# Kernel tuning notes

Hardware: AMD Instinct MI355X
Metric: run time of the kernel (lower is better)

The kernel has to match this reference:

```python
import jax, jax.numpy as jnp
import numpy as np

ALPHA = 0.5
EPS = 1e-6


def setup_inputs() -> dict:
    key = jax.random.key(0)
    k1, k2, k3 = jax.random.split(key, 3)
    B, N = 8192, 4096
    y_pred = jax.random.uniform(k1, (B, N), dtype=jnp.float32)
    y_true = jax.random.randint(k2, (B, N), 0, 2).astype(jnp.float32)
    depth_weights = jax.random.uniform(k3, (B, N), dtype=jnp.float32)
    return {"y_pred": y_pred, "y_true": y_true, "depth_weights": depth_weights}


def reference(y_pred, y_true, depth_weights):
    B, N = y_true.shape
    # --- weighted BCE ---
    bce = -(y_true * jnp.log(y_pred + EPS) + (1.0 - y_true) * jnp.log(1.0 - y_pred + EPS))
    wbce = jnp.mean(depth_weights * bce)

    # --- continuity-weighted loss: max run of correct predictions per row ---
    y_bin = (y_pred > 0.5).astype(y_true.dtype)
    correct = (y_bin == y_true)  # bool [B, N]
    idx = jnp.arange(N, dtype=jnp.int32)
    # position (1-based) of most recent incorrect element; 0 if none yet
    reset = jnp.where(correct, 0, idx + 1)  # [B, N]
    last_reset = jax.lax.cummax(reset, axis=1)  # [B, N]
    streak = (idx + 1)[None, :] - last_reset  # current run length at each position
    max_streak = jnp.max(streak, axis=1).astype(jnp.float32)  # [B]
    cwl = jnp.mean(1.0 - max_streak / N)

    return ALPHA * wbce + (1.0 - ALPHA) * cwl
```

## Files before the change

### kernel.cpp

```cpp
#include <hip/hip_runtime.h>

#define EPS 1e-6f
#define LN2F 0.69314718055994530942f

struct RunStats { int len, pre, suf, mx; };

__device__ inline RunStats rcombine(const RunStats& a, const RunStats& b) {
    RunStats r;
    r.len = a.len + b.len;
    r.pre = (a.pre == a.len) ? (a.len + b.pre) : a.pre;
    r.suf = (b.suf == b.len) ? (b.len + a.suf) : b.suf;
    r.mx  = max(max(a.mx, b.mx), a.suf + b.pre);
    return r;
}

__global__ __launch_bounds__(256) void row_kernel(
        const float* __restrict__ yp, const float* __restrict__ yt,
        const float* __restrict__ dw,
        float* __restrict__ row_wbce, int* __restrict__ row_streak) {
    const int row  = blockIdx.x;
    const int lane = threadIdx.x & 63;
    const int wave = threadIdx.x >> 6;
    const long base = (long)row * 4096 + wave * 1024 + lane * 4;

    const float4* pp = (const float4*)(yp + base);
    const float4* tp = (const float4*)(yt + base);
    const float4* wp = (const float4*)(dw + base);

    float4 P[4], T[4], W[4];
    #pragma unroll
    for (int q = 0; q < 4; ++q) {
        P[q] = pp[q * 64];
        T[q] = tp[q * 64];
        W[q] = wp[q * 64];
    }

    float sum = 0.0f;
    unsigned nibs = 0;
    #pragma unroll
    for (int q = 0; q < 4; ++q) {
        const float pv[4] = {P[q].x, P[q].y, P[q].z, P[q].w};
        const float tv[4] = {T[q].x, T[q].y, T[q].z, T[q].w};
        const float wv[4] = {W[q].x, W[q].y, W[q].z, W[q].w};
        #pragma unroll
        for (int c = 0; c < 4; ++c) {
            const bool tb = tv[c] != 0.0f;
            const float sel = tb ? pv[c] : 1.0f - pv[c];
            sum = fmaf(wv[c], __log2f(sel + EPS), sum);
            const bool correct = (pv[c] > 0.5f) == tb;
            nibs |= (unsigned)correct << (8 * q + c);
        }
    }

    __shared__ unsigned nibbuf[256];
    nibbuf[wave * 64 + lane] = nibs;
    __syncthreads();
    const uint4 d = *(const uint4*)&nibbuf[wave * 64 + 4 * (lane & 15)];
    const int qs = (lane >> 4) * 8;
    const unsigned mask = ((d.x >> qs) & 0xFu)
                        | (((d.y >> qs) & 0xFu) << 4)
                        | (((d.z >> qs) & 0xFu) << 8)
                        | (((d.w >> qs) & 0xFu) << 12);

    const int pre = __builtin_ctz(~mask);
    const int suf = __builtin_clz(~(mask << 16));
    int mx;
    {
        const unsigned p1 = mask;
        const unsigned p2 = p1 & (p1 << 1);
        const unsigned p4 = p2 & (p2 << 2);
        const unsigned p8 = p4 & (p4 << 4);
        unsigned z; int len;
        if (p8)      { z = p8; len = 8; }
        else if (p4) { z = p4; len = 4; }
        else if (p2) { z = p2; len = 2; }
        else         { z = p1; len = 1; }
        { const unsigned t = (z << 8) & p8; if (t) { z = t; len += 8; } }
        { const unsigned t = (z << 4) & p4; if (t) { z = t; len += 4; } }
        { const unsigned t = (z << 2) & p2; if (t) { z = t; len += 2; } }
        { const unsigned t = (z << 1) & p1; if (t) { z = t; len += 1; } }
        mx = mask ? len : 0;
    }

    #pragma unroll
    for (int off = 32; off; off >>= 1) sum += __shfl_down(sum, off);

    int packed = pre | (suf << 10) | (mx << 20);
    int alen = 16;
    #pragma unroll
    for (int off = 1; off < 32; off <<= 1) {
        const int o = __shfl_down(packed, off);
        const int apre = packed & 1023, asuf = (packed >> 10) & 1023, amx = packed >> 20;
        const int bpre = o & 1023,      bsuf = (o >> 10) & 1023,      bmx = o >> 20;
        const int npre = (apre == alen) ? (alen + bpre) : apre;
        const int nsuf = (bsuf == alen) ? (alen + asuf) : bsuf;
        const int nmx  = max(max(amx, bmx), asuf + bpre);
        packed = npre | (nsuf << 10) | (nmx << 20);
        alen <<= 1;
    }
    RunStats g;
    {
        const int o = __shfl_down(packed, 32);
        const int apre = packed & 1023, asuf = (packed >> 10) & 1023, amx = packed >> 20;
        const int bpre = o & 1023,      bsuf = (o >> 10) & 1023,      bmx = o >> 20;
        g.len = 1024;
        g.pre = (apre == 512) ? (512 + bpre) : apre;
        g.suf = (bsuf == 512) ? (512 + asuf) : bsuf;
        g.mx  = max(max(amx, bmx), asuf + bpre);
    }

    __shared__ RunStats sstat[4];
    __shared__ float ssum[4];
    if (lane == 0) { sstat[wave] = g; ssum[wave] = sum; }
    __syncthreads();
    if (threadIdx.x == 0) {
        RunStats r = rcombine(rcombine(sstat[0], sstat[1]), rcombine(sstat[2], sstat[3]));
        row_wbce[row]   = -LN2F * (ssum[0] + ssum[1] + ssum[2] + ssum[3]);
        row_streak[row] = r.mx;
    }
}

__global__ __launch_bounds__(1024) void finalize_kernel(
        const float* __restrict__ row_wbce, const int* __restrict__ row_streak,
        int rows, float* __restrict__ out) {
    double s = 0.0;
    long long st = 0;
    for (int i = threadIdx.x; i < rows; i += 1024) {
        s  += (double)row_wbce[i];
        st += (long long)row_streak[i];
    }
    __shared__ double sd[1024];
    __shared__ long long sl[1024];
    sd[threadIdx.x] = s; sl[threadIdx.x] = st;
    __syncthreads();
    for (int o = 512; o; o >>= 1) {
        if (threadIdx.x < o) {
            sd[threadIdx.x] += sd[threadIdx.x + o];
            sl[threadIdx.x] += sl[threadIdx.x + o];
        }
        __syncthreads();
    }
    if (threadIdx.x == 0) {
        const double total = (double)rows * 4096.0;
        const double wbce = sd[0] / total;
        const double cwl  = 1.0 - (double)sl[0] / total;
        out[0] = (float)(0.5 * wbce + 0.5 * cwl);
    }
}

extern "C" void kernel_launch(void* const* d_in, const int* in_sizes, int n_in,
                              void* d_out, int out_size, void* d_ws, size_t ws_size,
                              hipStream_t stream) {
    const float* yp = (const float*)d_in[0];
    const float* yt = (const float*)d_in[1];
    const float* dw = (const float*)d_in[2];
    float* out = (float*)d_out;

    const int rows = in_sizes[0] / 4096;
    float* row_wbce   = (float*)d_ws;
    int*   row_streak = (int*)((char*)d_ws + (size_t)rows * sizeof(float));

    row_kernel<<<rows, 256, 0, stream>>>(yp, yt, dw, row_wbce, row_streak);
    finalize_kernel<<<1, 1024, 0, stream>>>(row_wbce, row_streak, rows, out);
}
```

Measured before the change: 348.7 us.

## Process four rows per block with register double-buffered prefetch

Each block now handles four rows and prefetches the next row's float4 loads into a second register buffer while computing the current one. This cuts block count and per-row sync/reduction overhead and aims to keep more loads in flight. The per-row __syncthreads before reading the shared nibble buffer was removed, but each wave reads only its own slice of that buffer, so this should be safe within a wave. Register pressure doubles, with launch_bounds(256,4) added, which may cause spills or lower occupancy.

```diff
diff --git a/kernel.cpp b/kernel.cpp
--- a/kernel.cpp
+++ b/kernel.cpp
@@ -2,6 +2,7 @@
 
 #define EPS 1e-6f
 #define LN2F 0.69314718055994530942f
+#define RPB 4
 
 struct RunStats { int len, pre, suf, mx; };
 
@@ -14,120 +15,141 @@
     return r;
 }
 
-__global__ __launch_bounds__(256) void row_kernel(
+__global__ __launch_bounds__(256, 4) void row_kernel(
         const float* __restrict__ yp, const float* __restrict__ yt,
         const float* __restrict__ dw,
-        float* __restrict__ row_wbce, int* __restrict__ row_streak) {
-    const int row  = blockIdx.x;
+        float* __restrict__ blk_wbce, int* __restrict__ blk_streak) {
     const int lane = threadIdx.x & 63;
     const int wave = threadIdx.x >> 6;
-    const long base = (long)row * 4096 + wave * 1024 + lane * 4;
+    const long base = (long)blockIdx.x * (RPB * 4096) + wave * 1024 + lane * 4;
 
     const float4* pp = (const float4*)(yp + base);
     const float4* tp = (const float4*)(yt + base);
     const float4* wp = (const float4*)(dw + base);
 
-    float4 P[4], T[4], W[4];
+    __shared__ unsigned nibbuf[256];
+    __shared__ RunStats sstat[RPB][4];
+    __shared__ float ssum[4];
+
+    float4 Pb[2][4], Tb[2][4], Wb[2][4];
     #pragma unroll
     for (int q = 0; q < 4; ++q) {
-        P[q] = pp[q * 64];
-        T[q] = tp[q * 64];
-        W[q] = wp[q * 64];
+        Pb[0][q] = pp[q * 64];
+        Tb[0][q] = tp[q * 64];
+        Wb[0][q] = wp[q * 64];
     }
 
     float sum = 0.0f;
-    unsigned nibs = 0;
     #pragma unroll
-    for (int q = 0; q < 4; ++q) {
-        const float pv[4] = {P[q].x, P[q].y, P[q].z, P[q].w};
-        const float tv[4] = {T[q].x, T[q].y, T[q].z, T[q].w};
-        const float wv[4] = {W[q].x, W[q].y, W[q].z, W[q].w};
+    for (int r = 0; r < RPB; ++r) {
+        const int cur = r & 1, nxt = cur ^ 1;
+        if (r + 1 < RPB) {
+            #pragma unroll
+            for (int q = 0; q < 4; ++q) {
+                Pb[nxt][q] = pp[(r + 1) * 1024 + q * 64];
+                Tb[nxt][q] = tp[(r + 1) * 1024 + q * 64];
+                Wb[nxt][q] = wp[(r + 1) * 1024 + q * 64];
+            }
+        }
+
+        unsigned nibs = 0;
         #pragma unroll
-        for (int c = 0; c < 4; ++c) {
-            const bool tb = tv[c] != 0.0f;
-            const float sel = tb ? pv[c] : 1.0f - pv[c];
-            sum = fmaf(wv[c], __log2f(sel + EPS), sum);
-            const bool correct = (pv[c] > 0.5f) == tb;
-            nibs |= (unsigned)correct << (8 * q + c);
+        for (int q = 0; q < 4; ++q) {
+            const float pv[4] = {Pb[cur][q].x, Pb[cur][q].y, Pb[cur][q].z, Pb[cur][q].w};
+            const float tv[4] = {Tb[cur][q].x, Tb[cur][q].y, Tb[cur][q].z, Tb[cur][q].w};
+            const float wv[4] = {Wb[cur][q].x, Wb[cur][q].y, Wb[cur][q].z, Wb[cur][q].w};
+            #pragma unroll
+            for (int c = 0; c < 4; ++c) {
+                const bool tb = tv[c] != 0.0f;
+                const float sel = tb ? pv[c] : 1.0f - pv[c];
+                sum = fmaf(wv[c], __log2f(sel + EPS), sum);
+                const bool correct = (pv[c] > 0.5f) == tb;
+                nibs |= (unsigned)correct << (8 * q + c);
+            }
         }
-    }
 
-    __shared__ unsigned nibbuf[256];
-    nibbuf[wave * 64 + lane] = nibs;
-    __syncthreads();
-    const uint4 d = *(const uint4*)&nibbuf[wave * 64 + 4 * (lane & 15)];
-    const int qs = (lane >> 4) * 8;
-    const unsigned mask = ((d.x >> qs) & 0xFu)
-                        | (((d.y >> qs) & 0xFu) << 4)
-                        | (((d.z >> qs) & 0xFu) << 8)
-                        | (((d.w >> qs) & 0xFu) << 12);
+        nibbuf[wave * 64 + lane] = nibs;
+        const uint4 d = *(const uint4*)&nibbuf[wave * 64 + 4 * (lane & 15)];
+        const int qs = (lane >> 4) * 8;
+        const unsigned mask = ((d.x >> qs) & 0xFu)
+                            | (((d.y >> qs) & 0xFu) << 4)
+                            | (((d.z >> qs) & 0xFu) << 8)
+                            | (((d.w >> qs) & 0xFu) << 12);
 
-    const int pre = __builtin_ctz(~mask);
-    const int suf = __builtin_clz(~(mask << 16));
-    int mx;
-    {
-        const unsigned p1 = mask;
-        const unsigned p2 = p1 & (p1 << 1);
-        const unsigned p4 = p2 & (p2 << 2);
-        const unsigned p8 = p4 & (p4 << 4);
-        unsigned z; int len;
-        if (p8)      { z = p8; len = 8; }
-        else if (p4) { z = p4; len = 4; }
-        else if (p2) { z = p2; len = 2; }
-        else         { z = p1; len = 1; }
-        { const unsigned t = (z << 8) & p8; if (t) { z = t; len += 8; } }
-        { const unsigned t = (z << 4) & p4; if (t) { z = t; len += 4; } }
-        { const unsigned t = (z << 2) & p2; if (t) { z = t; len += 2; } }
-        { const unsigned t = (z << 1) & p1; if (t) { z = t; len += 1; } }
-        mx = mask ? len : 0;
+        const int pre = __builtin_ctz(~mask);
+        const int suf = __builtin_clz(~(mask << 16));
+        int mx;
+        {
+            const unsigned p1 = mask;
+            const unsigned p2 = p1 & (p1 << 1);
+            const unsigned p4 = p2 & (p2 << 2);
+            const unsigned p8 = p4 & (p4 << 4);
+            unsigned z; int len;
+            if (p8)      { z = p8; len = 8; }
+            else if (p4) { z = p4; len = 4; }
+            else if (p2) { z = p2; len = 2; }
+            else         { z = p1; len = 1; }
+            { const unsigned t = (z << 8) & p8; if (t) { z = t; len += 8; } }
+            { const unsigned t = (z << 4) & p4; if (t) { z = t; len += 4; } }
+            { const unsigned t = (z << 2) & p2; if (t) { z = t; len += 2; } }
+            { const unsigned t = (z << 1) & p1; if (t) { z = t; len += 1; } }
+            mx = mask ? len : 0;
+        }
+
+        int packed = pre | (suf << 10) | (mx << 20);
+        int alen = 16;
+        #pragma unroll
+        for (int off = 1; off < 32; off <<= 1) {
+            const int o = __shfl_down(packed, off);
+            const int apre = packed & 1023, asuf = (packed >> 10) & 1023, amx = packed >> 20;
+            const int bpre = o & 1023,      bsuf = (o >> 10) & 1023,      bmx = o >> 20;
+            const int npre = (apre == alen) ? (alen + bpre) : apre;
+            const int nsuf = (bsuf == alen) ? (alen + asuf) : bsuf;
+            const int nmx  = max(max(amx, bmx), asuf + bpre);
+            packed = npre | (nsuf << 10) | (nmx << 20);
+            alen <<= 1;
+        }
+        {
+            const int o = __shfl_down(packed, 32);
+            const int apre = packed & 1023, asuf = (packed >> 10) & 1023, amx = packed >> 20;
+            const int bpre = o & 1023,      bsuf = (o >> 10) & 1023,      bmx = o >> 20;
+            if (lane == 0) {
+                RunStats g;
+                g.len = 1024;
+                g.pre = (apre == 512) ? (512 + bpre) : apre;
+                g.suf = (bsuf == 512) ? (512 + asuf) : bsuf;
+                g.mx  = max(max(amx, bmx), asuf + bpre);
+                sstat[r][wave] = g;
+            }
+        }
     }
 
     #pragma unroll
     for (int off = 32; off; off >>= 1) sum += __shfl_down(sum, off);
+    if (lane == 0) ssum[wave] = sum;
 
-    int packed = pre | (suf << 10) | (mx << 20);
-    int alen = 16;
-    #pragma unroll
-    for (int off = 1; off < 32; off <<= 1) {
-        const int o = __shfl_down(packed, off);
-        const int apre = packed & 1023, asuf = (packed >> 10) & 1023, amx = packed >> 20;
-        const int bpre = o & 1023,      bsuf = (o >> 10) & 1023,      bmx = o >> 20;
-        const int npre = (apre == alen) ? (alen + bpre) : apre;
-        const int nsuf = (bsuf == alen) ? (alen + asuf) : bsuf;
-        const int nmx  = max(max(amx, bmx), asuf + bpre);
-        packed = npre | (nsuf << 10) | (nmx << 20);
-        alen <<= 1;
-    }
-    RunStats g;
-    {
-        const int o = __shfl_down(packed, 32);
-        const int apre = packed & 1023, asuf = (packed >> 10) & 1023, amx = packed >> 20;
-        const int bpre = o & 1023,      bsuf = (o >> 10) & 1023,      bmx = o >> 20;
-        g.len = 1024;
-        g.pre = (apre == 512) ? (512 + bpre) : apre;
-        g.suf = (bsuf == 512) ? (512 + asuf) : bsuf;
-        g.mx  = max(max(amx, bmx), asuf + bpre);
-    }
-
-    __shared__ RunStats sstat[4];
-    __shared__ float ssum[4];
-    if (lane == 0) { sstat[wave] = g; ssum[wave] = sum; }
     __syncthreads();
     if (threadIdx.x == 0) {
-        RunStats r = rcombine(rcombine(sstat[0], sstat[1]), rcombine(sstat[2], sstat[3]));
-        row_wbce[row]   = -LN2F * (ssum[0] + ssum[1] + ssum[2] + ssum[3]);
-        row_streak[row] = r.mx;
+        int stot = 0;
+        #pragma unroll
+        for (int r = 0; r < RPB; ++r) {
+            RunStats c = rcombine(rcombine(sstat[r][0], sstat[r][1]),
+                                  rcombine(sstat[r][2], sstat[r][3]));
+            stot += c.mx;
+        }
+        blk_wbce[blockIdx.x]   = -LN2F * (ssum[0] + ssum[1] + ssum[2] + ssum[3]);
+        blk_streak[blockIdx.x] = stot;
     }
 }
 
 __global__ __launch_bounds__(1024) void finalize_kernel(
-        const float* __restrict__ row_wbce, const int* __restrict__ row_streak,
-        int rows, float* __restrict__ out) {
+        const float* __restrict__ blk_wbce, const int* __restrict__ blk_streak,
+        int nblk, int rows, float* __restrict__ out) {
     double s = 0.0;
     long long st = 0;
-    for (int i = threadIdx.x; i < rows; i += 1024) {
-        s  += (double)row_wbce[i];
-        st += (long long)row_streak[i];
+    for (int i = threadIdx.x; i < nblk; i += 1024) {
+        s  += (double)blk_wbce[i];
+        st += (long long)blk_streak[i];
     }
     __shared__ double sd[1024];
     __shared__ long long sl[1024];
@@ -157,9 +179,10 @@
     float* out = (float*)d_out;
 
     const int rows = in_sizes[0] / 4096;
-    float* row_wbce   = (float*)d_ws;
-    int*   row_streak = (int*)((char*)d_ws + (size_t)rows * sizeof(float));
+    const int nblk = rows / RPB;
+    float* blk_wbce   = (float*)d_ws;
+    int*   blk_streak = (int*)((char*)d_ws + (size_t)nblk * sizeof(float));
 
-    row_kernel<<<rows, 256, 0, stream>>>(yp, yt, dw, row_wbce, row_streak);
-    finalize_kernel<<<1, 1024, 0, stream>>>(row_wbce, row_streak, rows, out);
+    row_kernel<<<nblk, 256, 0, stream>>>(yp, yt, dw, blk_wbce, blk_streak);
+    finalize_kernel<<<1, 1024, 0, stream>>>(blk_wbce, blk_streak, nblk, rows, out);
 }
```

Result: slower. 374.1 us (+7.3%).
